# Performance work log

Hardware: AMD Instinct MI355X
Metric: run time of the kernel (lower is better)

Reference implementation:

```python
import jax, jax.numpy as jnp
import numpy as np

VOCAB, EMB, LAYERS, OUT, N = 32000, 43, 64, 15, 524288

def setup_inputs() -> dict:
    key = jax.random.key(0)
    ks = jax.random.split(key, 8)
    emb = jax.random.normal(ks[0], (VOCAB, EMB), jnp.float32) * 0.1
    emb = emb.at[0].set(0.0)  # padding_idx=0
    return {
        "tokens": jax.random.randint(ks[1], (N,), 0, VOCAB, jnp.int32),
        "emb": emb,
        "w_ih": jax.random.normal(ks[2], (LAYERS, 4 * EMB, EMB), jnp.float32) * 0.1,
        "w_hh": jax.random.normal(ks[3], (LAYERS, 4 * EMB, EMB), jnp.float32) * 0.1,
        "b_ih": jax.random.normal(ks[4], (LAYERS, 4 * EMB), jnp.float32) * 0.1,
        "b_hh": jax.random.normal(ks[5], (LAYERS, 4 * EMB), jnp.float32) * 0.1,
        "w_out": jax.random.normal(ks[6], (OUT, EMB), jnp.float32) * 0.1,
        "b_out": jax.random.normal(ks[7], (OUT,), jnp.float32) * 0.1,
    }

def reference(tokens, emb, w_ih, w_hh, b_ih, b_hh, w_out, b_out):
    # embedding lookup; dropout is identity in eval mode
    x = emb[tokens]  # (N, EMB)

    # 64-layer LSTM stack, seq_len=1, h0=c0=0 => f-gate * c_prev and W_hh @ h_prev vanish,
    # but we implement the full PyTorch LSTM cell math (gate order i, f, g, o).
    def layer(h, params):
        wi, wh, bi, bh = params
        h_prev = jnp.zeros_like(h)  # initial hidden state per layer
        gates = h @ wi.T + bi + h_prev @ wh.T + bh  # (N, 4*EMB)
        i, f, g, o = jnp.split(gates, 4, axis=-1)
        c = jax.nn.sigmoid(f) * 0.0 + jax.nn.sigmoid(i) * jnp.tanh(g)
        h_new = jax.nn.sigmoid(o) * jnp.tanh(c)
        return h_new, None

    h, _ = jax.lax.scan(layer, x, (w_ih, w_hh, b_ih, b_hh))
    logits = h @ w_out.T + b_out  # (N, OUT)
    return jax.nn.log_softmax(logits, axis=1)
```

## Files before the change

kernel.cpp:

```cpp
#include <hip/hip_runtime.h>

#define LAYERS 64
#define EMBD   43
#define NOUT   15
#define NTOK   524288

#define MBLK    256
#define THREADS 256

#define ROWB      96
#define WROWS     144
#define IMGBYTES  (WROWS * ROWB)
#define IMGSTRIDE 14336
#define NCHUNK    14

#define HSBYTES   (MBLK * ROWB)
#define ZOFF      (HSBYTES + IMGSTRIDE)
#define SBYTES    (ZOFF + 16)

#define NEG_L2E   -1.44269504f
#define NEG_2L2E  -2.88539008f

typedef short bf16x8 __attribute__((ext_vector_type(8)));
typedef float f32x4  __attribute__((ext_vector_type(4)));
typedef float f32x2  __attribute__((ext_vector_type(2)));

__device__ __forceinline__ unsigned short f2bf(float f) {
  unsigned int u = __builtin_bit_cast(unsigned int, f);
  u = u + 0x7fffu + ((u >> 16) & 1u);
  return (unsigned short)(u >> 16);
}
__device__ __forceinline__ float bf2f(unsigned short s) {
  unsigned int u = ((unsigned int)s) << 16;
  return __builtin_bit_cast(float, u);
}

__device__ __forceinline__ int slotbyte(int g, int row) {
  return (g < 4) ? (((g + (row >> 2)) & 3) * 16)
                 : (64 + (((g - 4) ^ ((row >> 2) & 1)) * 16));
}

__global__ void pack_w_kernel(const float* __restrict__ w_ih,
                              const float* __restrict__ b_ih,
                              const float* __restrict__ b_hh,
                              unsigned char* __restrict__ wpack) {
  int idx = blockIdx.x * blockDim.x + threadIdx.x;
  if (idx >= LAYERS * WROWS) return;
  int l = idx / WROWS, n = idx % WROWS;
  int t = n >> 4, c = n & 15;
  int G = t / 3, gidx = t % 3;
  int gsel = (gidx == 0) ? 0 : ((gidx == 1) ? 2 : 3);
  float scale = (gidx == 1) ? NEG_2L2E : NEG_L2E;
  int j = (G == 0) ? 2 * c : ((G == 1) ? 2 * c + 1 : 32 + c);
  int valid = (j < EMBD);
  const float* src = w_ih + ((size_t)l * 172 + (size_t)gsel * EMBD + j) * EMBD;
  float bias = 0.0f;
  if (valid) {
    int R = gsel * EMBD + j;
    bias = (b_ih[l * 172 + R] + b_hh[l * 172 + R]) * scale;
  }
  unsigned char* dst = wpack + (size_t)l * IMGSTRIDE + n * ROWB;
  #pragma unroll
  for (int g = 0; g < 6; ++g) {
    union { unsigned short s[8]; uint4 v; } pk;
    #pragma unroll
    for (int e = 0; e < 8; ++e) {
      int k = g * 8 + e;
      unsigned short val = 0;
      if (valid && k < EMBD) val = f2bf(src[k] * scale);
      else if (valid && k == EMBD) val = f2bf(bias);
      pk.s[e] = val;
    }
    *(uint4*)(dst + slotbyte(g, n)) = pk.v;
  }
}

__global__ void __launch_bounds__(THREADS, 4) lstm_kernel(
    const int* __restrict__ tokens,
    const float* __restrict__ emb,
    const unsigned char* __restrict__ wpack,
    const float* __restrict__ w_out,
    const float* __restrict__ b_out,
    float* __restrict__ out) {
  __shared__ __align__(16) unsigned char S[SBYTES];

  const int tid  = threadIdx.x;
  const int lane = tid & 63;
  const int wave = tid >> 6;
  const int c    = lane & 15;
  const int q    = lane >> 4;
  const int row_base = blockIdx.x * MBLK;

  {
    const unsigned char* src = wpack;
    #pragma unroll
    for (int ch = 0; ch < 4; ++ch) {
      int chunk = wave + ch * 4;
      if (chunk < NCHUNK)
        __builtin_amdgcn_global_load_lds(
            (const __attribute__((address_space(1))) void*)(src + chunk * 1024 + lane * 16),
            (__attribute__((address_space(3))) void*)(S + HSBYTES + chunk * 1024),
            16, 0, 0);
    }
  }

  {
    int r = tid;
    int tok = tokens[row_base + r];
    const float* e = emb + (size_t)tok * EMBD;
    unsigned short v[48];
    #pragma unroll
    for (int k = 0; k < EMBD; ++k) v[k] = f2bf(e[k]);
    v[EMBD] = 0x3F80;
    #pragma unroll
    for (int k = EMBD + 1; k < 48; ++k) v[k] = 0;
    #pragma unroll
    for (int g = 0; g < 6; ++g) {
      union { unsigned short s[8]; uint4 u; } pk;
      #pragma unroll
      for (int e2 = 0; e2 < 8; ++e2) pk.s[e2] = v[g * 8 + e2];
      *(uint4*)(S + r * ROWB + slotbyte(g, r)) = pk.u;
    }
    if (tid == 0) {
      uint4 z4 = {0u, 0u, 0u, 0u};
      *(uint4*)(S + ZOFF) = z4;
    }
  }

  int adrA0, adrA1, adrB0, adrB1, incHi, adrP[4], adrSg[4];
  {
    int ra = wave * 64 + c;
    adrA0 = ra * ROWB + (((q + (c >> 2)) & 3) * 16);
    adrB0 = HSBYTES + c * ROWB + (((q + (c >> 2)) & 3) * 16);
    if (q < 2) {
      adrA1 = ra * ROWB + 64 + ((q ^ ((c >> 2) & 1)) * 16);
      adrB1 = HSBYTES + c * ROWB + 64 + ((q ^ ((c >> 2) & 1)) * 16);
      incHi = 16 * ROWB;
    } else {
      adrA1 = ZOFF;
      adrB1 = ZOFF;
      incHi = 0;
    }
    #pragma unroll
    for (int r4 = 0; r4 < 4; ++r4) {
      int rr = wave * 64 + q * 4 + r4;
      adrP[r4]  = rr * ROWB + ((((c >> 2) + q) & 3) * 16) + (c & 3) * 4;
      adrSg[r4] = rr * ROWB + 64 + (((c >> 3) ^ (q & 1)) * 16) + (c & 7) * 2;
    }
  }
  __syncthreads();

  const f32x4 zf = {0.0f, 0.0f, 0.0f, 0.0f};

  #pragma unroll 1
  for (int l = 0; l < LAYERS; ++l) {
    bf16x8 A0[4], A1[4];
    {
      int a1 = adrA1;
      #pragma unroll
      for (int st = 0; st < 4; ++st) {
        A0[st] = *(const bf16x8*)(S + adrA0 + st * (16 * ROWB));
        A1[st] = *(const bf16x8*)(S + a1);
        a1 += incHi;
      }
    }

    float hh[16];
    int b1 = adrB1;

    #pragma unroll
    for (int G = 0; G < 3; ++G) {
      f32x4 acc[3][4];
      #pragma unroll
      for (int t2 = 0; t2 < 3; ++t2) {
        int off = (G * 3 + t2) * (16 * ROWB);
        bf16x8 B0 = *(const bf16x8*)(S + adrB0 + off);
        #pragma unroll
        for (int st = 0; st < 4; ++st)
          acc[t2][st] = __builtin_amdgcn_mfma_f32_16x16x32_bf16(A0[st], B0, zf, 0, 0, 0);
      }
      #pragma unroll
      for (int t2 = 0; t2 < 3; ++t2) {
        bf16x8 B1 = *(const bf16x8*)(S + b1);
        b1 += incHi;
        #pragma unroll
        for (int st = 0; st < 4; ++st)
          acc[t2][st] = __builtin_amdgcn_mfma_f32_16x16x32_bf16(A1[st], B1, acc[t2][st], 0, 0, 0);
      }

      if (G == 2) {
        __syncthreads();
        if (l + 1 < LAYERS) {
          const unsigned char* src = wpack + (size_t)(l + 1) * IMGSTRIDE;
          #pragma unroll
          for (int ch = 0; ch < 4; ++ch) {
            int chunk = wave + ch * 4;
            if (chunk < NCHUNK)
              __builtin_amdgcn_global_load_lds(
                  (const __attribute__((address_space(1))) void*)(src + chunk * 1024 + lane * 16),
                  (__attribute__((address_space(3))) void*)(S + HSBYTES + chunk * 1024),
                  16, 0, 0);
          }
        }
      }

      #pragma unroll
      for (int st = 0; st < 4; ++st) {
        #pragma unroll
        for (int hp = 0; hp < 2; ++hp) {
          const int r0 = hp * 2, r1 = hp * 2 + 1;
          f32x2 t1, t2v, t3;
          t1[0]  = __builtin_amdgcn_exp2f(acc[0][st][r0]);
          t1[1]  = __builtin_amdgcn_exp2f(acc[0][st][r1]);
          t2v[0] = __builtin_amdgcn_exp2f(acc[1][st][r0]);
          t2v[1] = __builtin_amdgcn_exp2f(acc[1][st][r1]);
          t3[0]  = __builtin_amdgcn_exp2f(acc[2][st][r0]);
          t3[1]  = __builtin_amdgcn_exp2f(acc[2][st][r1]);
          const f32x2 one = {1.0f, 1.0f};
          const f32x2 two = {2.0f, 2.0f};
          const f32x2 k15 = {15.0f, 15.0f};
          const f32x2 k25 = {2.5f, 2.5f};
          const f32x2 k6  = {6.0f, 6.0f};
          f32x2 u   = t2v + one;
          f32x2 Qd  = __builtin_elementwise_fma(t1, u, u);
          f32x2 P   = two - u;
          f32x2 x   = P * P;
          f32x2 y   = Qd * Qd;
          f32x2 n1  = __builtin_elementwise_fma(y, k15, x);
          f32x2 dt  = __builtin_elementwise_fma(y, k25, x);
          f32x2 nP  = P * n1;
          f32x2 dQ  = Qd * dt;
          f32x2 v6  = __builtin_elementwise_fma(t3, k6, k6);
          f32x2 den = dQ * v6;
          float h0 = nP[0] * __builtin_amdgcn_rcpf(den[0]);
          float h1 = nP[1] * __builtin_amdgcn_rcpf(den[1]);
          if (G == 0) {
            hh[st * 4 + r0] = h0;
            hh[st * 4 + r1] = h1;
          } else if (G == 1) {
            {
              unsigned int u0 = __builtin_bit_cast(unsigned int, hh[st * 4 + r0]) + 0x8000u;
              unsigned int u1 = __builtin_bit_cast(unsigned int, h0) + 0x8000u;
              unsigned int pk = __builtin_amdgcn_perm(u1, u0, 0x07060302u);
              *(unsigned int*)(S + adrP[r0] + st * (16 * ROWB)) = pk;
            }
            {
              unsigned int u0 = __builtin_bit_cast(unsigned int, hh[st * 4 + r1]) + 0x8000u;
              unsigned int u1 = __builtin_bit_cast(unsigned int, h1) + 0x8000u;
              unsigned int pk = __builtin_amdgcn_perm(u1, u0, 0x07060302u);
              *(unsigned int*)(S + adrP[r1] + st * (16 * ROWB)) = pk;
            }
          } else if (c <= 10) {
            unsigned int u1 = (__builtin_bit_cast(unsigned int, h0) + 0x8000u) >> 16;
            *(unsigned short*)(S + adrSg[r0] + st * (16 * ROWB)) = (unsigned short)u1;
            unsigned int u2 = (__builtin_bit_cast(unsigned int, h1) + 0x8000u) >> 16;
            *(unsigned short*)(S + adrSg[r1] + st * (16 * ROWB)) = (unsigned short)u2;
          }
        }
      }
    }
    __syncthreads();
  }

  {
    int r = tid;
    float h[EMBD];
    #pragma unroll
    for (int g = 0; g < 6; ++g) {
      union { uint4 u; unsigned short s[8]; } pk;
      pk.u = *(const uint4*)(S + r * ROWB + slotbyte(g, r));
      #pragma unroll
      for (int e2 = 0; e2 < 8; ++e2) {
        int k = g * 8 + e2;
        if (k < EMBD) h[k] = bf2f(pk.s[e2]);
      }
    }
    float logit[NOUT];
    #pragma unroll
    for (int o = 0; o < NOUT; ++o) {
      float sum = b_out[o];
      #pragma unroll
      for (int k = 0; k < EMBD; ++k) sum += w_out[o * EMBD + k] * h[k];
      logit[o] = sum;
    }
    float m = logit[0];
    #pragma unroll
    for (int o = 1; o < NOUT; ++o) m = fmaxf(m, logit[o]);
    float ss = 0.0f;
    #pragma unroll
    for (int o = 0; o < NOUT; ++o) ss += __expf(logit[o] - m);
    float lse = m + __logf(ss);
    float* dst = out + (size_t)(row_base + r) * NOUT;
    #pragma unroll
    for (int o = 0; o < NOUT; ++o) dst[o] = logit[o] - lse;
  }
}

extern "C" void kernel_launch(void* const* d_in, const int* in_sizes, int n_in,
                              void* d_out, int out_size, void* d_ws, size_t ws_size,
                              hipStream_t stream) {
  const int* tokens     = (const int*)d_in[0];
  const float* emb      = (const float*)d_in[1];
  const float* w_ih     = (const float*)d_in[2];
  const float* b_ih     = (const float*)d_in[4];
  const float* b_hh     = (const float*)d_in[5];
  const float* w_out    = (const float*)d_in[6];
  const float* b_out    = (const float*)d_in[7];
  float* out            = (float*)d_out;

  const size_t need = (size_t)LAYERS * IMGSTRIDE;
  unsigned char* wpack = (ws_size >= need) ? (unsigned char*)d_ws
                                           : (unsigned char*)d_in[3];

  pack_w_kernel<<<(LAYERS * WROWS + 255) / 256, 256, 0, stream>>>(w_ih, b_ih, b_hh, wpack);
  lstm_kernel<<<NTOK / MBLK, THREADS, 0, stream>>>(tokens, emb, wpack, w_out, b_out, out);
}
```

Baseline: 1.082 ms.

## Shrink LSTM row tile to 192 and use 128-byte XOR-swizzled hidden rows

```diff
diff --git a/kernel.cpp b/kernel.cpp
--- a/kernel.cpp
+++ b/kernel.cpp
@@ -5,16 +5,18 @@
 #define NOUT   15
 #define NTOK   524288
 
-#define MBLK    256
+#define MBLK    192
 #define THREADS 256
-
-#define ROWB      96
+#define NBLOCKS ((NTOK + MBLK - 1) / MBLK)
+
+#define HROWB     128
+#define WROWB     96
 #define WROWS     144
-#define IMGBYTES  (WROWS * ROWB)
+#define IMGBYTES  (WROWS * WROWB)
 #define IMGSTRIDE 14336
 #define NCHUNK    14
 
-#define HSBYTES   (MBLK * ROWB)
+#define HSBYTES   (MBLK * HROWB)
 #define ZOFF      (HSBYTES + IMGSTRIDE)
 #define SBYTES    (ZOFF + 16)
 
@@ -35,7 +37,7 @@
   return __builtin_bit_cast(float, u);
 }
 
-__device__ __forceinline__ int slotbyte(int g, int row) {
+__device__ __forceinline__ int wslot(int g, int row) {
   return (g < 4) ? (((g + (row >> 2)) & 3) * 16)
                  : (64 + (((g - 4) ^ ((row >> 2) & 1)) * 16));
 }
@@ -59,7 +61,7 @@
     int R = gsel * EMBD + j;
     bias = (b_ih[l * 172 + R] + b_hh[l * 172 + R]) * scale;
   }
-  unsigned char* dst = wpack + (size_t)l * IMGSTRIDE + n * ROWB;
+  unsigned char* dst = wpack + (size_t)l * IMGSTRIDE + n * WROWB;
   #pragma unroll
   for (int g = 0; g < 6; ++g) {
     union { unsigned short s[8]; uint4 v; } pk;
@@ -71,7 +73,7 @@
       else if (valid && k == EMBD) val = f2bf(bias);
       pk.s[e] = val;
     }
-    *(uint4*)(dst + slotbyte(g, n)) = pk.v;
+    *(uint4*)(dst + wslot(g, n)) = pk.v;
   }
 }
 
@@ -104,48 +106,50 @@
     }
   }
 
-  {
+  if (tid < MBLK) {
     int r = tid;
-    int tok = tokens[row_base + r];
+    int gr = row_base + r;
+    int tok = (gr < NTOK) ? tokens[gr] : 0;
     const float* e = emb + (size_t)tok * EMBD;
-    unsigned short v[48];
+    unsigned short v[64];
     #pragma unroll
     for (int k = 0; k < EMBD; ++k) v[k] = f2bf(e[k]);
     v[EMBD] = 0x3F80;
     #pragma unroll
-    for (int k = EMBD + 1; k < 48; ++k) v[k] = 0;
-    #pragma unroll
-    for (int g = 0; g < 6; ++g) {
+    for (int k = EMBD + 1; k < 64; ++k) v[k] = 0;
+    #pragma unroll
+    for (int g = 0; g < 8; ++g) {
       union { unsigned short s[8]; uint4 u; } pk;
       #pragma unroll
       for (int e2 = 0; e2 < 8; ++e2) pk.s[e2] = v[g * 8 + e2];
-      *(uint4*)(S + r * ROWB + slotbyte(g, r)) = pk.u;
-    }
-    if (tid == 0) {
-      uint4 z4 = {0u, 0u, 0u, 0u};
-      *(uint4*)(S + ZOFF) = z4;
-    }
+      *(uint4*)(S + r * HROWB + ((g ^ (r & 7)) * 16)) = pk.u;
+    }
+  }
+  if (tid == 0) {
+    uint4 z4 = {0u, 0u, 0u, 0u};
+    *(uint4*)(S + ZOFF) = z4;
   }
 
   int adrA0, adrA1, adrB0, adrB1, incHi, adrP[4], adrSg[4];
   {
-    int ra = wave * 64 + c;
-    adrA0 = ra * ROWB + (((q + (c >> 2)) & 3) * 16);
-    adrB0 = HSBYTES + c * ROWB + (((q + (c >> 2)) & 3) * 16);
+    int ra = wave * 48 + c;
+    adrA0 = ra * HROWB + ((q ^ (c & 7)) * 16);
+    adrA1 = ra * HROWB + (((4 + q) ^ (c & 7)) * 16);
+    adrB0 = HSBYTES + c * WROWB + (((q + (c >> 2)) & 3) * 16);
     if (q < 2) {
-      adrA1 = ra * ROWB + 64 + ((q ^ ((c >> 2) & 1)) * 16);
-      adrB1 = HSBYTES + c * ROWB + 64 + ((q ^ ((c >> 2) & 1)) * 16);
-      incHi = 16 * ROWB;
+      adrB1 = HSBYTES + c * WROWB + 64 + ((q ^ ((c >> 2) & 1)) * 16);
+      incHi = 16 * WROWB;
     } else {
-      adrA1 = ZOFF;
       adrB1 = ZOFF;
       incHi = 0;
     }
     #pragma unroll
     for (int r4 = 0; r4 < 4; ++r4) {
-      int rr = wave * 64 + q * 4 + r4;
-      adrP[r4]  = rr * ROWB + ((((c >> 2) + q) & 3) * 16) + (c & 3) * 4;
-      adrSg[r4] = rr * ROWB + 64 + (((c >> 3) ^ (q & 1)) * 16) + (c & 7) * 2;
+      int rq = q * 4 + r4;
+      int rm = rq & 7;
+      int rr = wave * 48 + rq;
+      adrP[r4]  = rr * HROWB + (((c >> 2) ^ rm) * 16) + (c & 3) * 4;
+      adrSg[r4] = rr * HROWB + (((4 + (c >> 3)) ^ rm) * 16) + (c & 7) * 2;
     }
   }
   __syncthreads();
@@ -154,29 +158,25 @@
 
   #pragma unroll 1
   for (int l = 0; l < LAYERS; ++l) {
-    bf16x8 A0[4], A1[4];
-    {
-      int a1 = adrA1;
-      #pragma unroll
-      for (int st = 0; st < 4; ++st) {
-        A0[st] = *(const bf16x8*)(S + adrA0 + st * (16 * ROWB));
-        A1[st] = *(const bf16x8*)(S + a1);
-        a1 += incHi;
-      }
-    }
-
-    float hh[16];
+    bf16x8 A0[3], A1[3];
+    #pragma unroll
+    for (int st = 0; st < 3; ++st) {
+      A0[st] = *(const bf16x8*)(S + adrA0 + st * (16 * HROWB));
+      A1[st] = *(const bf16x8*)(S + adrA1 + st * (16 * HROWB));
+    }
+
+    float hh[12];
     int b1 = adrB1;
 
     #pragma unroll
     for (int G = 0; G < 3; ++G) {
-      f32x4 acc[3][4];
+      f32x4 acc[3][3];
       #pragma unroll
       for (int t2 = 0; t2 < 3; ++t2) {
-        int off = (G * 3 + t2) * (16 * ROWB);
+        int off = (G * 3 + t2) * (16 * WROWB);
         bf16x8 B0 = *(const bf16x8*)(S + adrB0 + off);
         #pragma unroll
-        for (int st = 0; st < 4; ++st)
+        for (int st = 0; st < 3; ++st)
           acc[t2][st] = __builtin_amdgcn_mfma_f32_16x16x32_bf16(A0[st], B0, zf, 0, 0, 0);
       }
       #pragma unroll
@@ -184,7 +184,7 @@
         bf16x8 B1 = *(const bf16x8*)(S + b1);
         b1 += incHi;
         #pragma unroll
-        for (int st = 0; st < 4; ++st)
+        for (int st = 0; st < 3; ++st)
           acc[t2][st] = __builtin_amdgcn_mfma_f32_16x16x32_bf16(A1[st], B1, acc[t2][st], 0, 0, 0);
       }
 
@@ -205,7 +205,7 @@
       }
 
       #pragma unroll
-      for (int st = 0; st < 4; ++st) {
+      for (int st = 0; st < 3; ++st) {
         #pragma unroll
         for (int hp = 0; hp < 2; ++hp) {
           const int r0 = hp * 2, r1 = hp * 2 + 1;
@@ -242,19 +242,19 @@
               unsigned int u0 = __builtin_bit_cast(unsigned int, hh[st * 4 + r0]) + 0x8000u;
               unsigned int u1 = __builtin_bit_cast(unsigned int, h0) + 0x8000u;
               unsigned int pk = __builtin_amdgcn_perm(u1, u0, 0x07060302u);
-              *(unsigned int*)(S + adrP[r0] + st * (16 * ROWB)) = pk;
+              *(unsigned int*)(S + adrP[r0] + st * (16 * HROWB)) = pk;
             }
             {
               unsigned int u0 = __builtin_bit_cast(unsigned int, hh[st * 4 + r1]) + 0x8000u;
               unsigned int u1 = __builtin_bit_cast(unsigned int, h1) + 0x8000u;
               unsigned int pk = __builtin_amdgcn_perm(u1, u0, 0x07060302u);
-              *(unsigned int*)(S + adrP[r1] + st * (16 * ROWB)) = pk;
+              *(unsigned int*)(S + adrP[r1] + st * (16 * HROWB)) = pk;
             }
           } else if (c <= 10) {
             unsigned int u1 = (__builtin_bit_cast(unsigned int, h0) + 0x8000u) >> 16;
-            *(unsigned short*)(S + adrSg[r0] + st * (16 * ROWB)) = (unsigned short)u1;
+            *(unsigned short*)(S + adrSg[r0] + st * (16 * HROWB)) = (unsigned short)u1;
             unsigned int u2 = (__builtin_bit_cast(unsigned int, h1) + 0x8000u) >> 16;
-            *(unsigned short*)(S + adrSg[r1] + st * (16 * ROWB)) = (unsigned short)u2;
+            *(unsigned short*)(S + adrSg[r1] + st * (16 * HROWB)) = (unsigned short)u2;
           }
         }
       }
@@ -262,37 +262,40 @@
     __syncthreads();
   }
 
-  {
+  if (tid < MBLK) {
     int r = tid;
-    float h[EMBD];
-    #pragma unroll
-    for (int g = 0; g < 6; ++g) {
-      union { uint4 u; unsigned short s[8]; } pk;
-      pk.u = *(const uint4*)(S + r * ROWB + slotbyte(g, r));
-      #pragma unroll
-      for (int e2 = 0; e2 < 8; ++e2) {
-        int k = g * 8 + e2;
-        if (k < EMBD) h[k] = bf2f(pk.s[e2]);
-      }
-    }
-    float logit[NOUT];
-    #pragma unroll
-    for (int o = 0; o < NOUT; ++o) {
-      float sum = b_out[o];
-      #pragma unroll
-      for (int k = 0; k < EMBD; ++k) sum += w_out[o * EMBD + k] * h[k];
-      logit[o] = sum;
-    }
-    float m = logit[0];
-    #pragma unroll
-    for (int o = 1; o < NOUT; ++o) m = fmaxf(m, logit[o]);
-    float ss = 0.0f;
-    #pragma unroll
-    for (int o = 0; o < NOUT; ++o) ss += __expf(logit[o] - m);
-    float lse = m + __logf(ss);
-    float* dst = out + (size_t)(row_base + r) * NOUT;
-    #pragma unroll
-    for (int o = 0; o < NOUT; ++o) dst[o] = logit[o] - lse;
+    int gr = row_base + r;
+    if (gr < NTOK) {
+      float h[EMBD];
+      #pragma unroll
+      for (int g = 0; g < 6; ++g) {
+        union { uint4 u; unsigned short s[8]; } pk;
+        pk.u = *(const uint4*)(S + r * HROWB + ((g ^ (r & 7)) * 16));
+        #pragma unroll
+        for (int e2 = 0; e2 < 8; ++e2) {
+          int k = g * 8 + e2;
+          if (k < EMBD) h[k] = bf2f(pk.s[e2]);
+        }
+      }
+      float logit[NOUT];
+      #pragma unroll
+      for (int o = 0; o < NOUT; ++o) {
+        float sum = b_out[o];
+        #pragma unroll
+        for (int k = 0; k < EMBD; ++k) sum += w_out[o * EMBD + k] * h[k];
+        logit[o] = sum;
+      }
+      float m = logit[0];
+      #pragma unroll
+      for (int o = 1; o < NOUT; ++o) m = fmaxf(m, logit[o]);
+      float ss = 0.0f;
+      #pragma unroll
+      for (int o = 0; o < NOUT; ++o) ss += __expf(logit[o] - m);
+      float lse = m + __logf(ss);
+      float* dst = out + (size_t)gr * NOUT;
+      #pragma unroll
+      for (int o = 0; o < NOUT; ++o) dst[o] = logit[o] - lse;
+    }
   }
 }
 
@@ -313,5 +316,5 @@
                                            : (unsigned char*)d_in[3];
 
   pack_w_kernel<<<(LAYERS * WROWS + 255) / 256, 256, 0, stream>>>(w_ih, b_ih, b_hh, wpack);
-  lstm_kernel<<<NTOK / MBLK, THREADS, 0, stream>>>(tokens, emb, wpack, w_out, b_out, out);
-}
+  lstm_kernel<<<NBLOCKS, THREADS, 0, stream>>>(tokens, emb, wpack, w_out, b_out, out);
+}
```

Result: slower. 1.119 ms (+3.4%).

## Split LDS activation and weight rows into separate low/high K planes with new swizzle

Applied to the files above, without the earlier changes.

```diff
diff --git a/kernel.cpp b/kernel.cpp
--- a/kernel.cpp
+++ b/kernel.cpp
@@ -8,15 +8,14 @@
 #define MBLK    256
 #define THREADS 256
 
-#define ROWB      96
-#define WROWS     144
-#define IMGBYTES  (WROWS * ROWB)
+#define HLO   0
+#define HHI   16384
+#define WS    24576
+#define WHIO  9216
+#define ZOFF  38912
+#define SBYTES 38928
 #define IMGSTRIDE 14336
-#define NCHUNK    14
-
-#define HSBYTES   (MBLK * ROWB)
-#define ZOFF      (HSBYTES + IMGSTRIDE)
-#define SBYTES    (ZOFF + 16)
+#define NCHUNK 14
 
 #define NEG_L2E   -1.44269504f
 #define NEG_2L2E  -2.88539008f
@@ -35,9 +34,8 @@
   return __builtin_bit_cast(float, u);
 }
 
-__device__ __forceinline__ int slotbyte(int g, int row) {
-  return (g < 4) ? (((g + (row >> 2)) & 3) * 16)
-                 : (64 + (((g - 4) ^ ((row >> 2) & 1)) * 16));
+__device__ __forceinline__ int permrow(int n) {
+  return (n & ~5) | ((n & 1) << 2) | ((n >> 2) & 1);
 }
 
 __global__ void pack_w_kernel(const float* __restrict__ w_ih,
@@ -45,8 +43,8 @@
                               const float* __restrict__ b_hh,
                               unsigned char* __restrict__ wpack) {
   int idx = blockIdx.x * blockDim.x + threadIdx.x;
-  if (idx >= LAYERS * WROWS) return;
-  int l = idx / WROWS, n = idx % WROWS;
+  if (idx >= LAYERS * 144) return;
+  int l = idx / 144, n = idx % 144;
   int t = n >> 4, c = n & 15;
   int G = t / 3, gidx = t % 3;
   int gsel = (gidx == 0) ? 0 : ((gidx == 1) ? 2 : 3);
@@ -59,19 +57,29 @@
     int R = gsel * EMBD + j;
     bias = (b_ih[l * 172 + R] + b_hh[l * 172 + R]) * scale;
   }
-  unsigned char* dst = wpack + (size_t)l * IMGSTRIDE + n * ROWB;
+  unsigned short v[48];
   #pragma unroll
-  for (int g = 0; g < 6; ++g) {
-    union { unsigned short s[8]; uint4 v; } pk;
-    #pragma unroll
-    for (int e = 0; e < 8; ++e) {
-      int k = g * 8 + e;
-      unsigned short val = 0;
-      if (valid && k < EMBD) val = f2bf(src[k] * scale);
-      else if (valid && k == EMBD) val = f2bf(bias);
-      pk.s[e] = val;
-    }
-    *(uint4*)(dst + slotbyte(g, n)) = pk.v;
+  for (int k = 0; k < 48; ++k) {
+    unsigned short val = 0;
+    if (valid && k < EMBD) val = f2bf(src[k] * scale);
+    else if (valid && k == EMBD) val = f2bf(bias);
+    v[k] = val;
+  }
+  unsigned char* img = wpack + (size_t)l * IMGSTRIDE;
+  #pragma unroll
+  for (int s = 0; s < 4; ++s) {
+    union { unsigned short s16[8]; uint4 u; } pk;
+    #pragma unroll
+    for (int e = 0; e < 8; ++e) pk.s16[e] = v[s * 8 + e];
+    *(uint4*)(img + n * 64 + (((s + ((n >> 1) & 3)) & 3) * 16)) = pk.u;
+  }
+  #pragma unroll
+  for (int s = 0; s < 2; ++s) {
+    union { unsigned short s16[8]; uint4 u; } pk;
+    #pragma unroll
+    for (int e = 0; e < 8; ++e) pk.s16[e] = v[32 + s * 8 + e];
+    *(uint4*)(img + WHIO + n * 32 +
+              (((s ^ (n & 1) ^ ((n >> 2) & 1)) & 1) * 16)) = pk.u;
   }
 }
 
@@ -99,7 +107,7 @@
       if (chunk < NCHUNK)
         __builtin_amdgcn_global_load_lds(
             (const __attribute__((address_space(1))) void*)(src + chunk * 1024 + lane * 16),
-            (__attribute__((address_space(3))) void*)(S + HSBYTES + chunk * 1024),
+            (__attribute__((address_space(3))) void*)(S + WS + chunk * 1024),
             16, 0, 0);
     }
   }
@@ -114,38 +122,57 @@
     v[EMBD] = 0x3F80;
     #pragma unroll
     for (int k = EMBD + 1; k < 48; ++k) v[k] = 0;
-    #pragma unroll
-    for (int g = 0; g < 6; ++g) {
-      union { unsigned short s[8]; uint4 u; } pk;
-      #pragma unroll
-      for (int e2 = 0; e2 < 8; ++e2) pk.s[e2] = v[g * 8 + e2];
-      *(uint4*)(S + r * ROWB + slotbyte(g, r)) = pk.u;
-    }
-    if (tid == 0) {
-      uint4 z4 = {0u, 0u, 0u, 0u};
-      *(uint4*)(S + ZOFF) = z4;
-    }
-  }
-
-  int adrA0, adrA1, adrB0, adrB1, incHi, adrP[4], adrSg[4];
+    int pr = permrow(r);
+    int hr = (r & 1) ^ ((r >> 3) & 1);
+    #pragma unroll
+    for (int s = 0; s < 4; ++s) {
+      union { unsigned short s16[8]; uint4 u; } pk;
+      #pragma unroll
+      for (int e2 = 0; e2 < 8; ++e2) pk.s16[e2] = v[s * 8 + e2];
+      *(uint4*)(S + HLO + pr * 64 + (((s + (r & 3)) & 3) * 16)) = pk.u;
+    }
+    #pragma unroll
+    for (int s = 0; s < 2; ++s) {
+      union { unsigned short s16[8]; uint4 u; } pk;
+      #pragma unroll
+      for (int e2 = 0; e2 < 8; ++e2) pk.s16[e2] = v[32 + s * 8 + e2];
+      *(uint4*)(S + HHI + pr * 32 + (((s ^ hr) & 1) * 16)) = pk.u;
+    }
+  }
+  if (tid == 0) {
+    uint4 z4 = {0u, 0u, 0u, 0u};
+    *(uint4*)(S + ZOFF) = z4;
+  }
+
+  int adrA0, adrA1, incA1, adrB0, adrB1, incB1, adrP[4], adrSg[4];
   {
-    int ra = wave * 64 + c;
-    adrA0 = ra * ROWB + (((q + (c >> 2)) & 3) * 16);
-    adrB0 = HSBYTES + c * ROWB + (((q + (c >> 2)) & 3) * 16);
+    int pc = permrow(c);
+    int hc = (c & 1) ^ ((c >> 3) & 1);
+    int ra = wave * 64 + pc;
+    adrA0 = HLO + ra * 64 + (((q + (c & 3)) & 3) * 16);
     if (q < 2) {
-      adrA1 = ra * ROWB + 64 + ((q ^ ((c >> 2) & 1)) * 16);
-      adrB1 = HSBYTES + c * ROWB + 64 + ((q ^ ((c >> 2) & 1)) * 16);
-      incHi = 16 * ROWB;
+      adrA1 = HHI + ra * 32 + (((q ^ hc) & 1) * 16);
+      incA1 = 16 * 32;
     } else {
       adrA1 = ZOFF;
+      incA1 = 0;
+    }
+    adrB0 = WS + c * 64 + (((q + ((c >> 1) & 3)) & 3) * 16);
+    if (q < 2) {
+      adrB1 = WS + WHIO + c * 32 + (((q ^ (c & 1) ^ ((c >> 2) & 1)) & 1) * 16);
+      incB1 = 16 * 32;
+    } else {
       adrB1 = ZOFF;
-      incHi = 0;
+      incB1 = 0;
     }
     #pragma unroll
     for (int r4 = 0; r4 < 4; ++r4) {
-      int rr = wave * 64 + q * 4 + r4;
-      adrP[r4]  = rr * ROWB + ((((c >> 2) + q) & 3) * 16) + (c & 3) * 4;
-      adrSg[r4] = rr * ROWB + 64 + (((c >> 3) ^ (q & 1)) * 16) + (c & 7) * 2;
+      int rq  = q * 4 + r4;
+      int prq = permrow(rq);
+      int rr  = wave * 64 + prq;
+      adrP[r4]  = HLO + rr * 64 + ((((c >> 2) + r4) & 3) * 16) + (c & 3) * 4;
+      adrSg[r4] = HHI + rr * 32 +
+                  ((((c >> 3) ^ (r4 & 1) ^ (q >> 1)) & 1) * 16) + (c & 7) * 2;
     }
   }
   __syncthreads();
@@ -159,9 +186,9 @@
       int a1 = adrA1;
       #pragma unroll
       for (int st = 0; st < 4; ++st) {
-        A0[st] = *(const bf16x8*)(S + adrA0 + st * (16 * ROWB));
+        A0[st] = *(const bf16x8*)(S + adrA0 + st * 1024);
         A1[st] = *(const bf16x8*)(S + a1);
-        a1 += incHi;
+        a1 += incA1;
       }
     }
 
@@ -173,7 +200,7 @@
       f32x4 acc[3][4];
       #pragma unroll
       for (int t2 = 0; t2 < 3; ++t2) {
-        int off = (G * 3 + t2) * (16 * ROWB);
+        int off = (G * 3 + t2) * 1024;
         bf16x8 B0 = *(const bf16x8*)(S + adrB0 + off);
         #pragma unroll
         for (int st = 0; st < 4; ++st)
@@ -182,7 +209,7 @@
       #pragma unroll
       for (int t2 = 0; t2 < 3; ++t2) {
         bf16x8 B1 = *(const bf16x8*)(S + b1);
-        b1 += incHi;
+        b1 += incB1;
         #pragma unroll
         for (int st = 0; st < 4; ++st)
           acc[t2][st] = __builtin_amdgcn_mfma_f32_16x16x32_bf16(A1[st], B1, acc[t2][st], 0, 0, 0);
@@ -198,7 +225,7 @@
             if (chunk < NCHUNK)
               __builtin_amdgcn_global_load_lds(
                   (const __attribute__((address_space(1))) void*)(src + chunk * 1024 + lane * 16),
-                  (__attribute__((address_space(3))) void*)(S + HSBYTES + chunk * 1024),
+                  (__attribute__((address_space(3))) void*)(S + WS + chunk * 1024),
                   16, 0, 0);
           }
         }
@@ -242,19 +269,19 @@
               unsigned int u0 = __builtin_bit_cast(unsigned int, hh[st * 4 + r0]) + 0x8000u;
               unsigned int u1 = __builtin_bit_cast(unsigned int, h0) + 0x8000u;
               unsigned int pk = __builtin_amdgcn_perm(u1, u0, 0x07060302u);
-              *(unsigned int*)(S + adrP[r0] + st * (16 * ROWB)) = pk;
+              *(unsigned int*)(S + adrP[r0] + st * 1024) = pk;
             }
             {
               unsigned int u0 = __builtin_bit_cast(unsigned int, hh[st * 4 + r1]) + 0x8000u;
               unsigned int u1 = __builtin_bit_cast(unsigned int, h1) + 0x8000u;
               unsigned int pk = __builtin_amdgcn_perm(u1, u0, 0x07060302u);
-              *(unsigned int*)(S + adrP[r1] + st * (16 * ROWB)) = pk;
+              *(unsigned int*)(S + adrP[r1] + st * 1024) = pk;
             }
           } else if (c <= 10) {
             unsigned int u1 = (__builtin_bit_cast(unsigned int, h0) + 0x8000u) >> 16;
-            *(unsigned short*)(S + adrSg[r0] + st * (16 * ROWB)) = (unsigned short)u1;
+            *(unsigned short*)(S + adrSg[r0] + st * 512) = (unsigned short)u1;
             unsigned int u2 = (__builtin_bit_cast(unsigned int, h1) + 0x8000u) >> 16;
-            *(unsigned short*)(S + adrSg[r1] + st * (16 * ROWB)) = (unsigned short)u2;
+            *(unsigned short*)(S + adrSg[r1] + st * 512) = (unsigned short)u2;
           }
         }
       }
@@ -264,15 +291,24 @@
 
   {
     int r = tid;
+    int pr = permrow(r);
+    int hr = (r & 1) ^ ((r >> 3) & 1);
     float h[EMBD];
     #pragma unroll
-    for (int g = 0; g < 6; ++g) {
-      union { uint4 u; unsigned short s[8]; } pk;
-      pk.u = *(const uint4*)(S + r * ROWB + slotbyte(g, r));
+    for (int s = 0; s < 4; ++s) {
+      union { uint4 u; unsigned short s16[8]; } pk;
+      pk.u = *(const uint4*)(S + HLO + pr * 64 + (((s + (r & 3)) & 3) * 16));
+      #pragma unroll
+      for (int e2 = 0; e2 < 8; ++e2) h[s * 8 + e2] = bf2f(pk.s16[e2]);
+    }
+    #pragma unroll
+    for (int s = 0; s < 2; ++s) {
+      union { uint4 u; unsigned short s16[8]; } pk;
+      pk.u = *(const uint4*)(S + HHI + pr * 32 + (((s ^ hr) & 1) * 16));
       #pragma unroll
       for (int e2 = 0; e2 < 8; ++e2) {
-        int k = g * 8 + e2;
-        if (k < EMBD) h[k] = bf2f(pk.s[e2]);
+        int k = 32 + s * 8 + e2;
+        if (k < EMBD) h[k] = bf2f(pk.s16[e2]);
       }
     }
     float logit[NOUT];
@@ -312,6 +348,6 @@
   unsigned char* wpack = (ws_size >= need) ? (unsigned char*)d_ws
                                            : (unsigned char*)d_in[3];
 
-  pack_w_kernel<<<(LAYERS * WROWS + 255) / 256, 256, 0, stream>>>(w_ih, b_ih, b_hh, wpack);
+  pack_w_kernel<<<(LAYERS * 144 + 255) / 256, 256, 0, stream>>>(w_ih, b_ih, b_hh, wpack);
   lstm_kernel<<<NTOK / MBLK, THREADS, 0, stream>>>(tokens, emb, wpack, w_out, b_out, out);
 }
```

New measurement: 1.091 ms. About the same (+0.8%).
